# Performance work log

Hardware: AMD Instinct MI355X
Metric: run time of the kernel (lower is better)

## Reference

```python
import jax, jax.numpy as jnp
import numpy as np

B, T, D_IN, P, Q, D_OUT = 128, 1024, 64, 128, 2, 64


def _lstm_layer(x, w_ih, w_hh, b):
    """One LSTM layer, batch_first. x: [B,T,Din], w_ih: [4P,Din], w_hh: [4P,P], b: [4P].
    PyTorch gate order: i, f, g, o."""
    # Precompute input contribution for all timesteps (the big, parallel GEMM).
    gx = jnp.einsum('btd,gd->btg', x, w_ih) + b          # [B,T,4P]
    gx_t = jnp.swapaxes(gx, 0, 1)                        # [T,B,4P] for scan
    p = w_hh.shape[1]
    h0 = jnp.zeros((x.shape[0], p), dtype=x.dtype)
    c0 = jnp.zeros((x.shape[0], p), dtype=x.dtype)

    def step(carry, g_in):
        h, c = carry
        g = g_in + h @ w_hh.T                            # [B,4P]
        i, f, gg, o = jnp.split(g, 4, axis=-1)
        i = jax.nn.sigmoid(i)
        f = jax.nn.sigmoid(f)
        gg = jnp.tanh(gg)
        o = jax.nn.sigmoid(o)
        c = f * c + i * gg
        h = o * jnp.tanh(c)
        return (h, c), h

    _, hs = jax.lax.scan(step, (h0, c0), gx_t)           # hs: [T,B,P]
    return jnp.swapaxes(hs, 0, 1)                        # [B,T,P]


def setup_inputs() -> dict:
    key = jax.random.key(0)
    ks = jax.random.split(key, 8)
    x = jax.random.normal(ks[0], (B, T, D_IN), dtype=jnp.float32)
    # weight_ih: kaiming-normal-ish; weight_hh: orthogonal-ish (random normal is a fine stand-in
    # numerically; init distribution doesn't change the math being tested).
    w_ih0 = jax.random.normal(ks[1], (4 * P, D_IN), dtype=jnp.float32) * (1.0 / np.sqrt(D_IN))
    w_hh0 = jax.random.normal(ks[2], (4 * P, P), dtype=jnp.float32) * (1.0 / np.sqrt(P))
    w_ih1 = jax.random.normal(ks[3], (4 * P, P), dtype=jnp.float32) * (1.0 / np.sqrt(P))
    w_hh1 = jax.random.normal(ks[4], (4 * P, P), dtype=jnp.float32) * (1.0 / np.sqrt(P))
    # biases initialized to zero in the original (bias_ih + bias_hh folded into one per layer
    # would be equivalent math; keep both for faithfulness)
    b_ih = jnp.zeros((Q, 4 * P), dtype=jnp.float32)
    b_hh = jnp.zeros((Q, 4 * P), dtype=jnp.float32)
    fc_w = jax.random.normal(ks[5], (D_OUT, P), dtype=jnp.float32) * np.sqrt(2.0 / P)
    fc_b = jnp.zeros((D_OUT,), dtype=jnp.float32)
    return {"x": x, "w_ih0": w_ih0, "w_hh0": w_hh0, "w_ih1": w_ih1, "w_hh1": w_hh1,
            "b_ih": b_ih, "b_hh": b_hh, "fc_w": fc_w, "fc_b": fc_b}


def reference(x, w_ih0, w_hh0, w_ih1, w_hh1, b_ih, b_hh, fc_w, fc_b):
    h = _lstm_layer(x, w_ih0, w_hh0, b_ih[0] + b_hh[0])   # layer 0: [B,T,P]
    h = _lstm_layer(h, w_ih1, w_hh1, b_ih[1] + b_hh[1])   # layer 1: [B,T,P]
    return jnp.einsum('btp,op->bto', h, fc_w) + fc_b      # [B,T,D_OUT]
```

## Files before the change

### kernel.cpp

```cpp
#include <hip/hip_runtime.h>

#define NT 1024
#define RINGS 256

typedef _Float16 half8 __attribute__((ext_vector_type(8)));
typedef _Float16 half4 __attribute__((ext_vector_type(4)));
typedef float f32x4 __attribute__((ext_vector_type(4)));
typedef unsigned long long u64;
struct U2 { u64 a, b; };

#ifndef __has_builtin
#define __has_builtin(x) 0
#endif

__device__ __forceinline__ f32x4 MFMA(half8 a, half8 b, f32x4 c) {
  return __builtin_amdgcn_mfma_f32_16x16x32_f16(a, b, c, 0, 0, 0);
}
__device__ __forceinline__ float exp2h(float x) {
#if __has_builtin(__builtin_amdgcn_exp2f)
  return __builtin_amdgcn_exp2f(x);
#else
  return exp2f(x);
#endif
}
__device__ __forceinline__ float sigf(float x) {
  return __builtin_amdgcn_rcpf(1.0f + exp2h(x * -1.44269504f));
}
__device__ __forceinline__ float tanhf2(float x) {
  float t = __builtin_amdgcn_rcpf(1.0f + exp2h(x * 2.88539008f));
  return fmaf(-2.0f, t, 1.0f);
}
__device__ __forceinline__ half8 cvt8(float4 c0, float4 c1) {
  half8 hv;
  hv[0] = (_Float16)c0.x; hv[1] = (_Float16)c0.y;
  hv[2] = (_Float16)c0.z; hv[3] = (_Float16)c0.w;
  hv[4] = (_Float16)c1.x; hv[5] = (_Float16)c1.y;
  hv[6] = (_Float16)c1.z; hv[7] = (_Float16)c1.w;
  return hv;
}
__device__ __forceinline__ half8 ldring(const _Float16* p) {
  const u64* q = (const u64*)p;
  U2 uu;
  uu.a = __hip_atomic_load(q, __ATOMIC_RELAXED, __HIP_MEMORY_SCOPE_AGENT);
  uu.b = __hip_atomic_load(q + 1, __ATOMIC_RELAXED, __HIP_MEMORY_SCOPE_AGENT);
  return __builtin_bit_cast(half8, uu);
}
__device__ __forceinline__ unsigned wpoll(unsigned* p, unsigned tgt,
                                          unsigned cached, int l) {
  unsigned c = cached;
  while (c < tgt) {
    unsigned pv = 0;
    if (l == 0)
      pv = __hip_atomic_load(p, __ATOMIC_ACQUIRE, __HIP_MEMORY_SCOPE_AGENT);
    c = (unsigned)__builtin_amdgcn_readfirstlane((int)pv);
    if (c < tgt) __builtin_amdgcn_s_sleep(2);
  }
  return c;
}

__global__ __launch_bounds__(256) void prep_x(const float* __restrict__ x,
                                              _Float16* __restrict__ Xf) {
  int t0 = blockIdx.x * 256 + threadIdx.x;
  int l = t0 & 63;
  int fid = t0 >> 6;
  int kt = fid & 1;
  int t = (fid >> 1) & (NT - 1);
  int g = fid >> 11;
  int bt = g * 16 + (l & 15);
  int kb = kt * 32 + (l >> 4) * 4;
  const float* src = x + ((size_t)bt * NT + (size_t)t) * 64 + kb;
  float4 v0 = *(const float4*)src;
  float4 v1 = *(const float4*)(src + 16);
  *(half8*)(Xf + (size_t)fid * 512 + l * 8) = cvt8(v0, v1);
}

__global__ __launch_bounds__(512, 1) void lstm_main(
    const float* __restrict__ wih0, const float* __restrict__ whh0,
    const float* __restrict__ wih1, const float* __restrict__ whh1,
    const float* __restrict__ bih, const float* __restrict__ bhh,
    const float* __restrict__ fcw, const float* __restrict__ fcb,
    const _Float16* __restrict__ Xf, _Float16* __restrict__ ringH0,
    unsigned* __restrict__ flags, float* __restrict__ out) {
  const int tid = threadIdx.x;
  const int w = tid >> 6, l = tid & 63;
  const int n = l & 15, lg = l >> 4;
  const bool producer = blockIdx.x < 8;
  const int g = blockIdx.x & 7;

  __shared__ _Float16 hfr[2][4][64][8];
  __shared__ _Float16 fcl[4][4][64][8];

  _Float16* ringG = ringH0 + (size_t)g * RINGS * 2048;
  unsigned* prog = flags + g * 16;
  unsigned* cons = flags + (8 + g) * 16;
  const half8 hz = {0, 0, 0, 0, 0, 0, 0, 0};

  if (producer) {
    half8 A[4][6];
    f32x4 bias[4];
#pragma unroll
    for (int q = 0; q < 4; ++q) {
      int row = (w + 8 * q) * 16 + n;
#pragma unroll
      for (int kt = 0; kt < 2; ++kt) {
        const float* wp = wih0 + (size_t)row * 64 + kt * 32 + lg * 4;
        A[q][kt] = cvt8(*(const float4*)wp, *(const float4*)(wp + 16));
      }
#pragma unroll
      for (int kt = 0; kt < 4; ++kt) {
        const float* wp = whh0 + (size_t)row * 128 + kt * 32 + lg * 4;
        A[q][2 + kt] = cvt8(*(const float4*)wp, *(const float4*)(wp + 16));
      }
      int rb = (w + 8 * q) * 16 + lg * 4;
      f32x4 bv;
#pragma unroll
      for (int r = 0; r < 4; ++r) bv[r] = bih[rb + r] + bhh[rb + r];
      bias[q] = bv;
    }
    if (tid < 256) ((half8*)&hfr[1][0][0][0])[tid] = hz;
    const _Float16* XfG = Xf + (size_t)g * NT * 1024;
    half8 x0 = *(const half8*)(XfG + l * 8);
    half8 x1 = *(const half8*)(XfG + 512 + l * 8);
    f32x4 cst = {0.f, 0.f, 0.f, 0.f};
    unsigned Cc = 0;
    __syncthreads();
    for (int s = 0; s < NT; ++s) {
      half8 xn0, xn1;
      if (s + 1 < NT) {
        const _Float16* p = XfG + (size_t)(s + 1) * 1024 + l * 8;
        xn0 = *(const half8*)p;
        xn1 = *(const half8*)(p + 512);
      }
      if (s >= 224 && (s & 31) == 0)
        Cc = wpoll(cons, (unsigned)(s - 192), Cc, l);
      const int rdk = (s + 1) & 1;
      half8 b2 = *(const half8*)&hfr[rdk][0][l][0];
      half8 b3 = *(const half8*)&hfr[rdk][1][l][0];
      half8 b4 = *(const half8*)&hfr[rdk][2][l][0];
      half8 b5 = *(const half8*)&hfr[rdk][3][l][0];
      f32x4 xc0 = {0.f, 0.f, 0.f, 0.f}, xc1 = xc0, xc2 = xc0, xc3 = xc0;
      xc0 = MFMA(A[0][0], x0, xc0); xc1 = MFMA(A[1][0], x0, xc1);
      xc2 = MFMA(A[2][0], x0, xc2); xc3 = MFMA(A[3][0], x0, xc3);
      xc0 = MFMA(A[0][1], x1, xc0); xc1 = MFMA(A[1][1], x1, xc1);
      xc2 = MFMA(A[2][1], x1, xc2); xc3 = MFMA(A[3][1], x1, xc3);
      f32x4 hc0 = bias[0], hc1 = bias[1], hc2 = bias[2], hc3 = bias[3];
      hc0 = MFMA(A[0][2], b2, hc0); hc1 = MFMA(A[1][2], b2, hc1);
      hc2 = MFMA(A[2][2], b2, hc2); hc3 = MFMA(A[3][2], b2, hc3);
      hc0 = MFMA(A[0][3], b3, hc0); hc1 = MFMA(A[1][3], b3, hc1);
      hc2 = MFMA(A[2][3], b3, hc2); hc3 = MFMA(A[3][3], b3, hc3);
      hc0 = MFMA(A[0][4], b4, hc0); hc1 = MFMA(A[1][4], b4, hc1);
      hc2 = MFMA(A[2][4], b4, hc2); hc3 = MFMA(A[3][4], b4, hc3);
      hc0 = MFMA(A[0][5], b5, hc0); hc1 = MFMA(A[1][5], b5, hc1);
      hc2 = MFMA(A[2][5], b5, hc2); hc3 = MFMA(A[3][5], b5, hc3);
      f32x4 acc0 = hc0 + xc0, acc1 = hc1 + xc1;
      f32x4 acc2 = hc2 + xc2, acc3 = hc3 + xc3;
      half4 hh;
#pragma unroll
      for (int r = 0; r < 4; ++r) {
        float iv = sigf(acc0[r]), fv = sigf(acc1[r]);
        float gv = tanhf2(acc2[r]), ov = sigf(acc3[r]);
        cst[r] = fv * cst[r] + iv * gv;
        hh[r] = (_Float16)(ov * tanhf2(cst[r]));
      }
      *(half4*)&hfr[s & 1][w >> 1][l][(w & 1) << 2] = hh;
      {
        u64 uh = __builtin_bit_cast(u64, hh);
        __hip_atomic_store(
            (u64*)(ringG + (size_t)(s & (RINGS - 1)) * 2048 +
                   (w >> 1) * 512 + l * 8 + (w & 1) * 4),
            uh, __ATOMIC_RELAXED, __HIP_MEMORY_SCOPE_AGENT);
      }
      asm volatile("s_waitcnt lgkmcnt(0)" ::: "memory");
      __builtin_amdgcn_sched_barrier(0);
      __builtin_amdgcn_s_barrier();
      __builtin_amdgcn_sched_barrier(0);
      if ((s & 31) == 31) {
        asm volatile("s_waitcnt vmcnt(0)" ::: "memory");
        __builtin_amdgcn_sched_barrier(0);
        __builtin_amdgcn_s_barrier();
        __builtin_amdgcn_sched_barrier(0);
        if (tid == 0)
          __hip_atomic_store(prog, (unsigned)(s + 1), __ATOMIC_RELEASE,
                             __HIP_MEMORY_SCOPE_AGENT);
      }
      x0 = xn0;
      x1 = xn1;
    }
  } else {
    half8 A[4][8];
    f32x4 bias[4], fcbv = {0.f, 0.f, 0.f, 0.f};
#pragma unroll
    for (int q = 0; q < 4; ++q) {
      int row = (w + 8 * q) * 16 + n;
#pragma unroll
      for (int kt = 0; kt < 4; ++kt) {
        const float* wp = wih1 + (size_t)row * 128 + kt * 32 + lg * 4;
        A[q][kt] = cvt8(*(const float4*)wp, *(const float4*)(wp + 16));
      }
#pragma unroll
      for (int kt = 0; kt < 4; ++kt) {
        const float* wp = whh1 + (size_t)row * 128 + kt * 32 + lg * 4;
        A[q][4 + kt] = cvt8(*(const float4*)wp, *(const float4*)(wp + 16));
      }
      int rb = (w + 8 * q) * 16 + lg * 4;
      f32x4 bv;
#pragma unroll
      for (int r = 0; r < 4; ++r)
        bv[r] = bih[512 + rb + r] + bhh[512 + rb + r];
      bias[q] = bv;
    }
    if (w < 4) {
      int frow = (w << 4) + n;
#pragma unroll
      for (int kt = 0; kt < 4; ++kt) {
        const float* wp = fcw + (size_t)frow * 128 + kt * 32 + lg * 4;
        *(half8*)&fcl[w][kt][l][0] =
            cvt8(*(const float4*)wp, *(const float4*)(wp + 16));
      }
      fcbv = *(const f32x4*)(fcb + (w << 4) + lg * 4);
    }
    if (tid < 256) ((half8*)&hfr[1][0][0][0])[tid] = hz;
    float* outG = out + (size_t)((g << 4) + n) * NT * 64 + (w << 4) + lg * 4;
    f32x4 cst = {0.f, 0.f, 0.f, 0.f};
    __syncthreads();
    unsigned Pc = wpoll(prog, 2u, 0u, l);
    half8 hA0 = ldring(ringG + l * 8);
    half8 hA1 = ldring(ringG + 512 + l * 8);
    half8 hA2 = ldring(ringG + 1024 + l * 8);
    half8 hA3 = ldring(ringG + 1536 + l * 8);
    const _Float16* rb1 = ringG + 2048 + l * 8;
    half8 hB0 = ldring(rb1);
    half8 hB1 = ldring(rb1 + 512);
    half8 hB2 = ldring(rb1 + 1024);
    half8 hB3 = ldring(rb1 + 1536);

#define CSTEP(T, C0, C1, C2, C3)                                               \
  {                                                                            \
    const int rdk_ = ((T) + 1) & 1;                                            \
    half8 b4 = *(const half8*)&hfr[rdk_][0][l][0];                             \
    half8 b5 = *(const half8*)&hfr[rdk_][1][l][0];                             \
    half8 b6 = *(const half8*)&hfr[rdk_][2][l][0];                             \
    half8 b7 = *(const half8*)&hfr[rdk_][3][l][0];                             \
                      \
    f32x4 ic0 = {0.f, 0.f, 0.f, 0.f}, ic1 = ic0, ic2 = ic0, ic3 = ic0;         \
    ic0 = MFMA(A[0][0], C0, ic0); ic1 = MFMA(A[1][0], C0, ic1);                \
    ic2 = MFMA(A[2][0], C0, ic2); ic3 = MFMA(A[3][0], C0, ic3);                \
    ic0 = MFMA(A[0][1], C1, ic0); ic1 = MFMA(A[1][1], C1, ic1);                \
    ic2 = MFMA(A[2][1], C1, ic2); ic3 = MFMA(A[3][1], C1, ic3);                \
    ic0 = MFMA(A[0][2], C2, ic0); ic1 = MFMA(A[1][2], C2, ic1);                \
    ic2 = MFMA(A[2][2], C2, ic2); ic3 = MFMA(A[3][2], C2, ic3);                \
    ic0 = MFMA(A[0][3], C3, ic0); ic1 = MFMA(A[1][3], C3, ic1);                \
    ic2 = MFMA(A[2][3], C3, ic2); ic3 = MFMA(A[3][3], C3, ic3);                \
    if ((T) + 2 < NT) {    \
      Pc = wpoll(prog, (unsigned)((T) + 3), Pc, l);                            \
      const _Float16* rb_ =                                                    \
          ringG + (size_t)(((T) + 2) & (RINGS - 1)) * 2048 + l * 8;            \
      C0 = ldring(rb_);        C1 = ldring(rb_ + 512);                         \
      C2 = ldring(rb_ + 1024); C3 = ldring(rb_ + 1536);                        \
    }                                                                          \
                                                   \
    f32x4 hc0 = bias[0], hc1 = bias[1], hc2 = bias[2], hc3 = bias[3];          \
    hc0 = MFMA(A[0][4], b4, hc0); hc1 = MFMA(A[1][4], b4, hc1);                \
    hc2 = MFMA(A[2][4], b4, hc2); hc3 = MFMA(A[3][4], b4, hc3);                \
    hc0 = MFMA(A[0][5], b5, hc0); hc1 = MFMA(A[1][5], b5, hc1);                \
    hc2 = MFMA(A[2][5], b5, hc2); hc3 = MFMA(A[3][5], b5, hc3);                \
    hc0 = MFMA(A[0][6], b6, hc0); hc1 = MFMA(A[1][6], b6, hc1);                \
    hc2 = MFMA(A[2][6], b6, hc2); hc3 = MFMA(A[3][6], b6, hc3);                \
    hc0 = MFMA(A[0][7], b7, hc0); hc1 = MFMA(A[1][7], b7, hc1);                \
    hc2 = MFMA(A[2][7], b7, hc2); hc3 = MFMA(A[3][7], b7, hc3);                \
    if (w < 4) {                           \
      half8 f0 = *(const half8*)&fcl[w][0][l][0];                              \
      half8 f1 = *(const half8*)&fcl[w][1][l][0];                              \
      half8 f2 = *(const half8*)&fcl[w][2][l][0];                              \
      half8 f3 = *(const half8*)&fcl[w][3][l][0];                              \
      f32x4 afc = fcbv;                                                        \
      afc = MFMA(f0, b4, afc); afc = MFMA(f1, b5, afc);                        \
      afc = MFMA(f2, b6, afc); afc = MFMA(f3, b7, afc);                        \
      if ((T) >= 1) *(f32x4*)(outG + (size_t)((T) - 1) * 64) = afc;            \
    }                                                                          \
    f32x4 acc0 = hc0 + ic0, acc1 = hc1 + ic1;                                  \
    f32x4 acc2 = hc2 + ic2, acc3 = hc3 + ic3;                                  \
    half4 hh;                                                                  \
    _Pragma("unroll")                                                          \
    for (int r = 0; r < 4; ++r) {                                              \
      float iv = sigf(acc0[r]), fv = sigf(acc1[r]);                            \
      float gv = tanhf2(acc2[r]), ov = sigf(acc3[r]);                          \
      cst[r] = fv * cst[r] + iv * gv;                                          \
      hh[r] = (_Float16)(ov * tanhf2(cst[r]));                                 \
    }                                                                          \
    *(half4*)&hfr[(T) & 1][w >> 1][l][(w & 1) << 2] = hh;                      \
    if (tid == 0 && ((T) & 31) == 0)                                           \
      __hip_atomic_store(cons, (unsigned)(T), __ATOMIC_RELAXED,                \
                         __HIP_MEMORY_SCOPE_AGENT);                            \
    asm volatile("s_waitcnt lgkmcnt(0)" ::: "memory");                         \
    __builtin_amdgcn_sched_barrier(0);                                         \
    __builtin_amdgcn_s_barrier();             \
    __builtin_amdgcn_sched_barrier(0);                                         \
  }

    for (int t = 0; t < NT; t += 2) {
      CSTEP(t, hA0, hA1, hA2, hA3);
      CSTEP(t + 1, hB0, hB1, hB2, hB3);
    }
#undef CSTEP
    {
      half8 b4 = *(const half8*)&hfr[(NT + 1) & 1][0][l][0];
      half8 b5 = *(const half8*)&hfr[(NT + 1) & 1][1][l][0];
      half8 b6 = *(const half8*)&hfr[(NT + 1) & 1][2][l][0];
      half8 b7 = *(const half8*)&hfr[(NT + 1) & 1][3][l][0];
      if (w < 4) {
        half8 f0 = *(const half8*)&fcl[w][0][l][0];
        half8 f1 = *(const half8*)&fcl[w][1][l][0];
        half8 f2 = *(const half8*)&fcl[w][2][l][0];
        half8 f3 = *(const half8*)&fcl[w][3][l][0];
        f32x4 afc = fcbv;
        afc = MFMA(f0, b4, afc); afc = MFMA(f1, b5, afc);
        afc = MFMA(f2, b6, afc); afc = MFMA(f3, b7, afc);
        *(f32x4*)(outG + (size_t)(NT - 1) * 64) = afc;
      }
    }
  }
}

extern "C" void kernel_launch(void* const* d_in, const int* in_sizes, int n_in,
                              void* d_out, int out_size, void* d_ws, size_t ws_size,
                              hipStream_t stream) {
  const float* x     = (const float*)d_in[0];
  const float* w_ih0 = (const float*)d_in[1];
  const float* w_hh0 = (const float*)d_in[2];
  const float* w_ih1 = (const float*)d_in[3];
  const float* w_hh1 = (const float*)d_in[4];
  const float* b_ih  = (const float*)d_in[5];
  const float* b_hh  = (const float*)d_in[6];
  const float* fc_w  = (const float*)d_in[7];
  const float* fc_b  = (const float*)d_in[8];

  _Float16* Xf   = (_Float16*)d_ws;
  _Float16* ring = (_Float16*)((char*)d_ws + (16u << 20));
  unsigned* flags = (unsigned*)((char*)d_ws + (24u << 20));

  hipMemsetAsync(flags, 0, 4096, stream);
  prep_x<<<4096, 256, 0, stream>>>(x, Xf);
  lstm_main<<<16, 512, 0, stream>>>(w_ih0, w_hh0, w_ih1, w_hh1, b_ih, b_hh,
                                    fc_w, fc_b, Xf, ring, flags,
                                    (float*)d_out);
}
```

Baseline: 1.337 ms.

## Precompute next step's input-gate MFMAs off the recurrent critical path

In both LSTM layers, the input-to-gate MFMA product for step t+1 (with bias folded in) is now computed during step t and used as the accumulator seed for the recurrent MFMAs. This removes the input MFMAs and the add from the serial h-dependency chain, so each step waits only on the recurrent MFMAs. The input loads are issued two steps ahead. The layer-1 two-step macro unroll is replaced by a plain loop, which adds live accumulator registers and extra prologue MFMAs.

```diff
diff --git a/kernel.cpp b/kernel.cpp
--- a/kernel.cpp
+++ b/kernel.cpp
@@ -119,18 +119,20 @@
     }
     if (tid < 256) ((half8*)&hfr[1][0][0][0])[tid] = hz;
     const _Float16* XfG = Xf + (size_t)g * NT * 1024;
+    f32x4 cst = {0.f, 0.f, 0.f, 0.f};
+    unsigned Cc = 0;
     half8 x0 = *(const half8*)(XfG + l * 8);
     half8 x1 = *(const half8*)(XfG + 512 + l * 8);
-    f32x4 cst = {0.f, 0.f, 0.f, 0.f};
-    unsigned Cc = 0;
+    f32x4 xs0 = MFMA(A[0][0], x0, bias[0]);
+    f32x4 xs1 = MFMA(A[1][0], x0, bias[1]);
+    f32x4 xs2 = MFMA(A[2][0], x0, bias[2]);
+    f32x4 xs3 = MFMA(A[3][0], x0, bias[3]);
+    xs0 = MFMA(A[0][1], x1, xs0); xs1 = MFMA(A[1][1], x1, xs1);
+    xs2 = MFMA(A[2][1], x1, xs2); xs3 = MFMA(A[3][1], x1, xs3);
+    half8 xC0 = *(const half8*)(XfG + 1024 + l * 8);
+    half8 xC1 = *(const half8*)(XfG + 1024 + 512 + l * 8);
     __syncthreads();
     for (int s = 0; s < NT; ++s) {
-      half8 xn0, xn1;
-      if (s + 1 < NT) {
-        const _Float16* p = XfG + (size_t)(s + 1) * 1024 + l * 8;
-        xn0 = *(const half8*)p;
-        xn1 = *(const half8*)(p + 512);
-      }
       if (s >= 224 && (s & 31) == 0)
         Cc = wpoll(cons, (unsigned)(s - 192), Cc, l);
       const int rdk = (s + 1) & 1;
@@ -138,27 +140,34 @@
       half8 b3 = *(const half8*)&hfr[rdk][1][l][0];
       half8 b4 = *(const half8*)&hfr[rdk][2][l][0];
       half8 b5 = *(const half8*)&hfr[rdk][3][l][0];
-      f32x4 xc0 = {0.f, 0.f, 0.f, 0.f}, xc1 = xc0, xc2 = xc0, xc3 = xc0;
-      xc0 = MFMA(A[0][0], x0, xc0); xc1 = MFMA(A[1][0], x0, xc1);
-      xc2 = MFMA(A[2][0], x0, xc2); xc3 = MFMA(A[3][0], x0, xc3);
-      xc0 = MFMA(A[0][1], x1, xc0); xc1 = MFMA(A[1][1], x1, xc1);
-      xc2 = MFMA(A[2][1], x1, xc2); xc3 = MFMA(A[3][1], x1, xc3);
-      f32x4 hc0 = bias[0], hc1 = bias[1], hc2 = bias[2], hc3 = bias[3];
-      hc0 = MFMA(A[0][2], b2, hc0); hc1 = MFMA(A[1][2], b2, hc1);
-      hc2 = MFMA(A[2][2], b2, hc2); hc3 = MFMA(A[3][2], b2, hc3);
+      f32x4 hc0 = MFMA(A[0][2], b2, xs0);
+      f32x4 hc1 = MFMA(A[1][2], b2, xs1);
+      f32x4 hc2 = MFMA(A[2][2], b2, xs2);
+      f32x4 hc3 = MFMA(A[3][2], b2, xs3);
       hc0 = MFMA(A[0][3], b3, hc0); hc1 = MFMA(A[1][3], b3, hc1);
       hc2 = MFMA(A[2][3], b3, hc2); hc3 = MFMA(A[3][3], b3, hc3);
       hc0 = MFMA(A[0][4], b4, hc0); hc1 = MFMA(A[1][4], b4, hc1);
       hc2 = MFMA(A[2][4], b4, hc2); hc3 = MFMA(A[3][4], b4, hc3);
       hc0 = MFMA(A[0][5], b5, hc0); hc1 = MFMA(A[1][5], b5, hc1);
       hc2 = MFMA(A[2][5], b5, hc2); hc3 = MFMA(A[3][5], b5, hc3);
-      f32x4 acc0 = hc0 + xc0, acc1 = hc1 + xc1;
-      f32x4 acc2 = hc2 + xc2, acc3 = hc3 + xc3;
+      if (s + 1 < NT) {
+        xs0 = MFMA(A[0][0], xC0, bias[0]);
+        xs1 = MFMA(A[1][0], xC0, bias[1]);
+        xs2 = MFMA(A[2][0], xC0, bias[2]);
+        xs3 = MFMA(A[3][0], xC0, bias[3]);
+        xs0 = MFMA(A[0][1], xC1, xs0); xs1 = MFMA(A[1][1], xC1, xs1);
+        xs2 = MFMA(A[2][1], xC1, xs2); xs3 = MFMA(A[3][1], xC1, xs3);
+      }
+      if (s + 2 < NT) {
+        const _Float16* p = XfG + (size_t)(s + 2) * 1024 + l * 8;
+        xC0 = *(const half8*)p;
+        xC1 = *(const half8*)(p + 512);
+      }
       half4 hh;
 #pragma unroll
       for (int r = 0; r < 4; ++r) {
-        float iv = sigf(acc0[r]), fv = sigf(acc1[r]);
-        float gv = tanhf2(acc2[r]), ov = sigf(acc3[r]);
+        float iv = sigf(hc0[r]), fv = sigf(hc1[r]);
+        float gv = tanhf2(hc2[r]), ov = sigf(hc3[r]);
         cst[r] = fv * cst[r] + iv * gv;
         hh[r] = (_Float16)(ov * tanhf2(cst[r]));
       }
@@ -183,8 +192,6 @@
           __hip_atomic_store(prog, (unsigned)(s + 1), __ATOMIC_RELEASE,
                              __HIP_MEMORY_SCOPE_AGENT);
       }
-      x0 = xn0;
-      x1 = xn1;
     }
   } else {
     half8 A[4][8];
@@ -224,85 +231,89 @@
     f32x4 cst = {0.f, 0.f, 0.f, 0.f};
     __syncthreads();
     unsigned Pc = wpoll(prog, 2u, 0u, l);
-    half8 hA0 = ldring(ringG + l * 8);
-    half8 hA1 = ldring(ringG + 512 + l * 8);
-    half8 hA2 = ldring(ringG + 1024 + l * 8);
-    half8 hA3 = ldring(ringG + 1536 + l * 8);
+    half8 t0 = ldring(ringG + l * 8);
+    half8 t1 = ldring(ringG + 512 + l * 8);
+    half8 t2 = ldring(ringG + 1024 + l * 8);
+    half8 t3 = ldring(ringG + 1536 + l * 8);
+    f32x4 is0 = MFMA(A[0][0], t0, bias[0]);
+    f32x4 is1 = MFMA(A[1][0], t0, bias[1]);
+    f32x4 is2 = MFMA(A[2][0], t0, bias[2]);
+    f32x4 is3 = MFMA(A[3][0], t0, bias[3]);
+    is0 = MFMA(A[0][1], t1, is0); is1 = MFMA(A[1][1], t1, is1);
+    is2 = MFMA(A[2][1], t1, is2); is3 = MFMA(A[3][1], t1, is3);
+    is0 = MFMA(A[0][2], t2, is0); is1 = MFMA(A[1][2], t2, is1);
+    is2 = MFMA(A[2][2], t2, is2); is3 = MFMA(A[3][2], t2, is3);
+    is0 = MFMA(A[0][3], t3, is0); is1 = MFMA(A[1][3], t3, is1);
+    is2 = MFMA(A[2][3], t3, is2); is3 = MFMA(A[3][3], t3, is3);
     const _Float16* rb1 = ringG + 2048 + l * 8;
-    half8 hB0 = ldring(rb1);
-    half8 hB1 = ldring(rb1 + 512);
-    half8 hB2 = ldring(rb1 + 1024);
-    half8 hB3 = ldring(rb1 + 1536);
-
-#define CSTEP(T, C0, C1, C2, C3)                                               \
-  {                                                                            \
-    const int rdk_ = ((T) + 1) & 1;                                            \
-    half8 b4 = *(const half8*)&hfr[rdk_][0][l][0];                             \
-    half8 b5 = *(const half8*)&hfr[rdk_][1][l][0];                             \
-    half8 b6 = *(const half8*)&hfr[rdk_][2][l][0];                             \
-    half8 b7 = *(const half8*)&hfr[rdk_][3][l][0];                             \
-                      \
-    f32x4 ic0 = {0.f, 0.f, 0.f, 0.f}, ic1 = ic0, ic2 = ic0, ic3 = ic0;         \
-    ic0 = MFMA(A[0][0], C0, ic0); ic1 = MFMA(A[1][0], C0, ic1);                \
-    ic2 = MFMA(A[2][0], C0, ic2); ic3 = MFMA(A[3][0], C0, ic3);                \
-    ic0 = MFMA(A[0][1], C1, ic0); ic1 = MFMA(A[1][1], C1, ic1);                \
-    ic2 = MFMA(A[2][1], C1, ic2); ic3 = MFMA(A[3][1], C1, ic3);                \
-    ic0 = MFMA(A[0][2], C2, ic0); ic1 = MFMA(A[1][2], C2, ic1);                \
-    ic2 = MFMA(A[2][2], C2, ic2); ic3 = MFMA(A[3][2], C2, ic3);                \
-    ic0 = MFMA(A[0][3], C3, ic0); ic1 = MFMA(A[1][3], C3, ic1);                \
-    ic2 = MFMA(A[2][3], C3, ic2); ic3 = MFMA(A[3][3], C3, ic3);                \
-    if ((T) + 2 < NT) {    \
-      Pc = wpoll(prog, (unsigned)((T) + 3), Pc, l);                            \
-      const _Float16* rb_ =                                                    \
-          ringG + (size_t)(((T) + 2) & (RINGS - 1)) * 2048 + l * 8;            \
-      C0 = ldring(rb_);        C1 = ldring(rb_ + 512);                         \
-      C2 = ldring(rb_ + 1024); C3 = ldring(rb_ + 1536);                        \
-    }                                                                          \
-                                                   \
-    f32x4 hc0 = bias[0], hc1 = bias[1], hc2 = bias[2], hc3 = bias[3];          \
-    hc0 = MFMA(A[0][4], b4, hc0); hc1 = MFMA(A[1][4], b4, hc1);                \
-    hc2 = MFMA(A[2][4], b4, hc2); hc3 = MFMA(A[3][4], b4, hc3);                \
-    hc0 = MFMA(A[0][5], b5, hc0); hc1 = MFMA(A[1][5], b5, hc1);                \
-    hc2 = MFMA(A[2][5], b5, hc2); hc3 = MFMA(A[3][5], b5, hc3);                \
-    hc0 = MFMA(A[0][6], b6, hc0); hc1 = MFMA(A[1][6], b6, hc1);                \
-    hc2 = MFMA(A[2][6], b6, hc2); hc3 = MFMA(A[3][6], b6, hc3);                \
-    hc0 = MFMA(A[0][7], b7, hc0); hc1 = MFMA(A[1][7], b7, hc1);                \
-    hc2 = MFMA(A[2][7], b7, hc2); hc3 = MFMA(A[3][7], b7, hc3);                \
-    if (w < 4) {                           \
-      half8 f0 = *(const half8*)&fcl[w][0][l][0];                              \
-      half8 f1 = *(const half8*)&fcl[w][1][l][0];                              \
-      half8 f2 = *(const half8*)&fcl[w][2][l][0];                              \
-      half8 f3 = *(const half8*)&fcl[w][3][l][0];                              \
-      f32x4 afc = fcbv;                                                        \
-      afc = MFMA(f0, b4, afc); afc = MFMA(f1, b5, afc);                        \
-      afc = MFMA(f2, b6, afc); afc = MFMA(f3, b7, afc);                        \
-      if ((T) >= 1) *(f32x4*)(outG + (size_t)((T) - 1) * 64) = afc;            \
-    }                                                                          \
-    f32x4 acc0 = hc0 + ic0, acc1 = hc1 + ic1;                                  \
-    f32x4 acc2 = hc2 + ic2, acc3 = hc3 + ic3;                                  \
-    half4 hh;                                                                  \
-    _Pragma("unroll")                                                          \
-    for (int r = 0; r < 4; ++r) {                                              \
-      float iv = sigf(acc0[r]), fv = sigf(acc1[r]);                            \
-      float gv = tanhf2(acc2[r]), ov = sigf(acc3[r]);                          \
-      cst[r] = fv * cst[r] + iv * gv;                                          \
-      hh[r] = (_Float16)(ov * tanhf2(cst[r]));                                 \
-    }                                                                          \
-    *(half4*)&hfr[(T) & 1][w >> 1][l][(w & 1) << 2] = hh;                      \
-    if (tid == 0 && ((T) & 31) == 0)                                           \
-      __hip_atomic_store(cons, (unsigned)(T), __ATOMIC_RELAXED,                \
-                         __HIP_MEMORY_SCOPE_AGENT);                            \
-    asm volatile("s_waitcnt lgkmcnt(0)" ::: "memory");                         \
-    __builtin_amdgcn_sched_barrier(0);                                         \
-    __builtin_amdgcn_s_barrier();             \
-    __builtin_amdgcn_sched_barrier(0);                                         \
-  }
-
-    for (int t = 0; t < NT; t += 2) {
-      CSTEP(t, hA0, hA1, hA2, hA3);
-      CSTEP(t + 1, hB0, hB1, hB2, hB3);
-    }
-#undef CSTEP
+    half8 HC0 = ldring(rb1);
+    half8 HC1 = ldring(rb1 + 512);
+    half8 HC2 = ldring(rb1 + 1024);
+    half8 HC3 = ldring(rb1 + 1536);
+    for (int t = 0; t < NT; ++t) {
+      const int rdk = (t + 1) & 1;
+      half8 b4 = *(const half8*)&hfr[rdk][0][l][0];
+      half8 b5 = *(const half8*)&hfr[rdk][1][l][0];
+      half8 b6 = *(const half8*)&hfr[rdk][2][l][0];
+      half8 b7 = *(const half8*)&hfr[rdk][3][l][0];
+      f32x4 hc0 = MFMA(A[0][4], b4, is0);
+      f32x4 hc1 = MFMA(A[1][4], b4, is1);
+      f32x4 hc2 = MFMA(A[2][4], b4, is2);
+      f32x4 hc3 = MFMA(A[3][4], b4, is3);
+      hc0 = MFMA(A[0][5], b5, hc0); hc1 = MFMA(A[1][5], b5, hc1);
+      hc2 = MFMA(A[2][5], b5, hc2); hc3 = MFMA(A[3][5], b5, hc3);
+      hc0 = MFMA(A[0][6], b6, hc0); hc1 = MFMA(A[1][6], b6, hc1);
+      hc2 = MFMA(A[2][6], b6, hc2); hc3 = MFMA(A[3][6], b6, hc3);
+      hc0 = MFMA(A[0][7], b7, hc0); hc1 = MFMA(A[1][7], b7, hc1);
+      hc2 = MFMA(A[2][7], b7, hc2); hc3 = MFMA(A[3][7], b7, hc3);
+      if (w < 4) {
+        half8 f0 = *(const half8*)&fcl[w][0][l][0];
+        half8 f1 = *(const half8*)&fcl[w][1][l][0];
+        half8 f2 = *(const half8*)&fcl[w][2][l][0];
+        half8 f3 = *(const half8*)&fcl[w][3][l][0];
+        f32x4 afc = fcbv;
+        afc = MFMA(f0, b4, afc); afc = MFMA(f1, b5, afc);
+        afc = MFMA(f2, b6, afc); afc = MFMA(f3, b7, afc);
+        if (t >= 1) *(f32x4*)(outG + (size_t)(t - 1) * 64) = afc;
+      }
+      if (t + 1 < NT) {
+        is0 = MFMA(A[0][0], HC0, bias[0]);
+        is1 = MFMA(A[1][0], HC0, bias[1]);
+        is2 = MFMA(A[2][0], HC0, bias[2]);
+        is3 = MFMA(A[3][0], HC0, bias[3]);
+        is0 = MFMA(A[0][1], HC1, is0); is1 = MFMA(A[1][1], HC1, is1);
+        is2 = MFMA(A[2][1], HC1, is2); is3 = MFMA(A[3][1], HC1, is3);
+        is0 = MFMA(A[0][2], HC2, is0); is1 = MFMA(A[1][2], HC2, is1);
+        is2 = MFMA(A[2][2], HC2, is2); is3 = MFMA(A[3][2], HC2, is3);
+        is0 = MFMA(A[0][3], HC3, is0); is1 = MFMA(A[1][3], HC3, is1);
+        is2 = MFMA(A[2][3], HC3, is2); is3 = MFMA(A[3][3], HC3, is3);
+      }
+      if (t + 2 < NT) {
+        Pc = wpoll(prog, (unsigned)(t + 3), Pc, l);
+        const _Float16* rb_ =
+            ringG + (size_t)((t + 2) & (RINGS - 1)) * 2048 + l * 8;
+        HC0 = ldring(rb_);
+        HC1 = ldring(rb_ + 512);
+        HC2 = ldring(rb_ + 1024);
+        HC3 = ldring(rb_ + 1536);
+      }
+      half4 hh;
+#pragma unroll
+      for (int r = 0; r < 4; ++r) {
+        float iv = sigf(hc0[r]), fv = sigf(hc1[r]);
+        float gv = tanhf2(hc2[r]), ov = sigf(hc3[r]);
+        cst[r] = fv * cst[r] + iv * gv;
+        hh[r] = (_Float16)(ov * tanhf2(cst[r]));
+      }
+      *(half4*)&hfr[t & 1][w >> 1][l][(w & 1) << 2] = hh;
+      if (tid == 0 && (t & 31) == 0)
+        __hip_atomic_store(cons, (unsigned)t, __ATOMIC_RELAXED,
+                           __HIP_MEMORY_SCOPE_AGENT);
+      asm volatile("s_waitcnt lgkmcnt(0)" ::: "memory");
+      __builtin_amdgcn_sched_barrier(0);
+      __builtin_amdgcn_s_barrier();
+      __builtin_amdgcn_sched_barrier(0);
+    }
     {
       half8 b4 = *(const half8*)&hfr[(NT + 1) & 1][0][l][0];
       half8 b5 = *(const half8*)&hfr[(NT + 1) & 1][1][l][0];
```

Result: no change. 1.328 ms (-0.7%).
